# Performance work log

Hardware: AMD Instinct MI355X
Metric: run time of the kernel (lower is better)

Reference implementation:

```python
import jax, jax.numpy as jnp
import numpy as np
import math

FACTOR = 5  # ProbAttention factor default


def setup_inputs() -> dict:
    key = jax.random.key(0)
    k1, k2, k3, k4 = jax.random.split(key, 4)
    B, L, S, H, D = 4, 2048, 2048, 8, 64
    sample_k = min(FACTOR * math.ceil(math.log(L)), S)  # = 40
    return {
        "queries": jax.random.normal(k1, (B, L, H, D), dtype=jnp.float32),
        "keys": jax.random.normal(k2, (B, S, H, D), dtype=jnp.float32),
        "values": jax.random.normal(k3, (B, S, H, D), dtype=jnp.float32),
        # torch.randint(0, L_keys, (L_queries, sample_k)) hoisted out for determinism
        "index_sample": jax.random.randint(k4, (L, sample_k), 0, S, dtype=jnp.int32),
    }


def reference(queries, keys, values, index_sample):
    B, L, H, D = queries.shape
    S = keys.shape[1]
    # [B, H, L, D] layout as in forward's transpose(1, 2)
    q = jnp.transpose(queries, (0, 2, 1, 3))
    k = jnp.transpose(keys, (0, 2, 1, 3))
    v = jnp.transpose(values, (0, 2, 1, 3))

    n_top = min(FACTOR * math.ceil(math.log(S)) if S > 1 else 1, L)
    scale = 1.0 / math.sqrt(D)

    # --- _prob_QK ---
    # sampled keys per query position: [B, H, L, u, D]
    k_samp = k[:, :, index_sample, :]
    qk_sample = jnp.einsum('bhld,bhlud->bhlu', q, k_samp)  # [B, H, L, u]
    # sparsity measure M = max - mean (sum divided by full key length S)
    M = qk_sample.max(axis=-1) - qk_sample.sum(axis=-1) / S  # [B, H, L]
    M_top = jax.lax.top_k(M, n_top)[1]  # [B, H, n_top] query indices
    q_red = jnp.take_along_axis(q, M_top[..., None], axis=2)  # [B, H, n_top, D]
    scores = jnp.einsum('bhnd,bhsd->bhns', q_red, k) * scale  # [B, H, n_top, S]

    # --- softmax over keys (dropout p=0 -> identity) ---
    attn = jax.nn.softmax(scores, axis=-1)

    # --- initial context = mean of V, then scatter-update selected queries ---
    ctx_top = jnp.einsum('bhns,bhsd->bhnd', attn, v)  # [B, H, n_top, D]
    context = jnp.broadcast_to(v.mean(axis=2, keepdims=True), (B, H, L, D))
    bi = jnp.arange(B)[:, None, None]
    hi = jnp.arange(H)[None, :, None]
    context = context.at[bi, hi, M_top].set(ctx_top)

    return jnp.transpose(context, (0, 2, 1, 3))  # [B, L, H, D]
```

## Files before the change

### kernel.cpp

```cpp
#include <hip/hip_runtime.h>
#include <math.h>

constexpr int B = 4, L = 2048, S = 2048, H = 8, D = 64;
constexpr int U  = 40;
constexpr int NT = 40;
constexpr float SCALE = 0.125f;

__global__ void k_M_meanvpart(const float* __restrict__ q, const float* __restrict__ k,
                              const float* __restrict__ v, const int* __restrict__ idx,
                              float* __restrict__ M, float* __restrict__ part) {
    int tid = threadIdx.x;
    if (blockIdx.x < 2048) {
        int wid = tid >> 6, lane = tid & 63;
        int b = blockIdx.x & 3;
        int l = (blockIdx.x >> 2) * 4 + wid;
        int h = lane >> 3, dg = lane & 7;

        const float4* qr = (const float4*)(q + ((size_t)(b * L + l) * H + h) * D + dg * 8);
        float4 q0 = qr[0], q1 = qr[1];

        const int* irow = idx + l * U;
        const float* kb = k + (size_t)b * S * H * D + (size_t)h * D + dg * 8;
        float vmax = -INFINITY, vsum = 0.f;
#pragma unroll 4
        for (int u = 0; u < U; u++) {
            int s = irow[u];
            const float4* kr = (const float4*)(kb + (size_t)s * H * D);
            float4 k0 = kr[0], k1 = kr[1];
            float acc = q0.x * k0.x + q0.y * k0.y + q0.z * k0.z + q0.w * k0.w
                      + q1.x * k1.x + q1.y * k1.y + q1.z * k1.z + q1.w * k1.w;
            acc += __shfl_xor(acc, 1);
            acc += __shfl_xor(acc, 2);
            acc += __shfl_xor(acc, 4);
            vmax = fmaxf(vmax, acc);
            vsum += acc;
        }
        if (dg == 0) M[(size_t)(b * H + h) * L + l] = vmax - vsum / (float)S;
    } else {
        int blk = blockIdx.x - 2048;
        int b = blk >> 5, c = blk & 31;
        const float* p = v + ((size_t)(b * S + c * 64)) * 512;
        float a0 = 0.f, a1 = 0.f;
#pragma unroll
        for (int s = 0; s < 64; s++) {
            a0 += p[(size_t)s * 512 + tid];
            a1 += p[(size_t)s * 512 + tid + 256];
        }
        part[(size_t)blk * 512 + tid]       = a0;
        part[(size_t)blk * 512 + tid + 256] = a1;
    }
}

__device__ inline unsigned int fkey(float f) {
    unsigned int u = __float_as_uint(f);
    return (u & 0x80000000u) ? ~u : (u | 0x80000000u);
}

__global__ void k_topk_meanv(const float* __restrict__ M, int* __restrict__ topidx,
                             const float* __restrict__ part, float* __restrict__ meanv) {
    int tid = threadIdx.x;
    if (blockIdx.x >= 32) {
        int b = blockIdx.x - 32;
        float a0 = 0.f, a1 = 0.f;
#pragma unroll
        for (int c = 0; c < 32; c++) {
            a0 += part[(size_t)(b * 32 + c) * 512 + tid];
            a1 += part[(size_t)(b * 32 + c) * 512 + tid + 256];
        }
        meanv[b * 512 + tid]       = a0 * (1.f / (float)S);
        meanv[b * 512 + tid + 256] = a1 * (1.f / (float)S);
        return;
    }
    int bh = blockIdx.x;
    const float* m = M + (size_t)bh * L;

    __shared__ int hist[256];
    __shared__ unsigned int prefix_s;
    __shared__ int c_above_s, nsel_s, ntie_s, r_s;
    __shared__ int tie_i[L];

    unsigned int o[8];
    const float4* mr = (const float4*)(m + tid * 8);
    float4 a0 = mr[0], a1 = mr[1];
    o[0] = fkey(a0.x); o[1] = fkey(a0.y); o[2] = fkey(a0.z); o[3] = fkey(a0.w);
    o[4] = fkey(a1.x); o[5] = fkey(a1.y); o[6] = fkey(a1.z); o[7] = fkey(a1.w);

    if (tid == 0) { prefix_s = 0u; c_above_s = 0; nsel_s = 0; ntie_s = 0; }

    for (int sh = 24; sh >= 0; sh -= 8) {
        hist[tid] = 0;
        __syncthreads();
        unsigned int pfx = prefix_s;
#pragma unroll
        for (int j = 0; j < 8; j++) {
            bool match = (sh == 24) || ((o[j] >> (sh + 8)) == (pfx >> (sh + 8)));
            if (match) atomicAdd(&hist[(o[j] >> sh) & 0xFF], 1);
        }
        __syncthreads();
        if (tid < 64) {
            int4 hv = *(const int4*)&hist[tid * 4];
            int lsum = hv.x + hv.y + hv.z + hv.w;
            int s = lsum;
#pragma unroll
            for (int off = 1; off < 64; off <<= 1) {
                int t = __shfl_down(s, off);
                if (tid + off < 64) s += t;
            }
            int tail = s - lsum;
            int acc = c_above_s;
            int need = NT - acc;
            int t3 = tail + hv.w;
            int t2 = t3 + hv.z;
            int t1 = t2 + hv.y;
            int t0 = t1 + hv.x;
            if (t0 >= need && t1 < need) { prefix_s |= (unsigned)(4 * tid + 0) << sh; c_above_s = acc + t1; }
            else if (t1 >= need && t2 < need) { prefix_s |= (unsigned)(4 * tid + 1) << sh; c_above_s = acc + t2; }
            else if (t2 >= need && t3 < need) { prefix_s |= (unsigned)(4 * tid + 2) << sh; c_above_s = acc + t3; }
            else if (t3 >= need && tail < need) { prefix_s |= (unsigned)(4 * tid + 3) << sh; c_above_s = acc + tail; }
        }
        __syncthreads();
    }

    unsigned int T = prefix_s;

#pragma unroll
    for (int j = 0; j < 8; j++) {
        if (o[j] > T) {
            int slot = atomicAdd(&nsel_s, 1);
            topidx[bh * NT + slot] = tid * 8 + j;
        } else if (o[j] == T) {
            int p = atomicAdd(&ntie_s, 1);
            tie_i[p] = tid * 8 + j;
        }
    }
    __syncthreads();
    if (tid == 0) r_s = NT - nsel_s;
    __syncthreads();
    int r = r_s, ntie = ntie_s;

#pragma unroll
    for (int j = 0; j < 8; j++) {
        if (o[j] == T) {
            int myidx = tid * 8 + j;
            int rank = 0;
            for (int p = 0; p < ntie; p++) rank += (tie_i[p] < myidx) ? 1 : 0;
            if (rank < r) {
                int slot = atomicAdd(&nsel_s, 1);
                topidx[bh * NT + slot] = myidx;
            }
        }
    }
}

template <int NCH_>
__global__ __launch_bounds__(512) void k_attn_fill(
        const float* __restrict__ q, const float* __restrict__ k,
        const float* __restrict__ v, const int* __restrict__ topidx,
        const float* __restrict__ meanv,
        float* __restrict__ pctx, float* __restrict__ pm, float* __restrict__ pl,
        float4* __restrict__ out4) {
    constexpr int CS_ = S / NCH_;
    constexpr int CPL = CS_ / 128;
    int blk = blockIdx.x;
    int bh = blk / NCH_, c = blk % NCH_;
    int b = bh / H, h = bh % H;
    int s0 = c * CS_;
    int tid = threadIdx.x;
    int lane = tid & 63, g = tid >> 6;

    __shared__ float q_s[NT][D];
    __shared__ float p_s[NT][CS_ + 4];
    __shared__ float m_c[NT];

    for (int i = tid; i < NT * D; i += 512) {
        int n = i >> 6, d = i & 63;
        int lsel = topidx[bh * NT + n];
        q_s[n][d] = q[((size_t)(b * L + lsel) * H + h) * D + d];
    }
    __syncthreads();

    int rg = g & 3, ch = g >> 2;
    int r0 = rg * 10;
    int lc = ch * (CS_ / 2) + lane * CPL;
    const float* kp = k + ((size_t)(b * S + s0 + lc) * H + h) * D;

    float sc[10][CPL];
#pragma unroll
    for (int j = 0; j < 10; j++)
#pragma unroll
        for (int p = 0; p < CPL; p++) sc[j][p] = 0.f;

#pragma unroll
    for (int dc = 0; dc < 64; dc += 16) {
        float4 kf[CPL][4];
#pragma unroll
        for (int p = 0; p < CPL; p++) {
            const float* kc = kp + (size_t)p * H * D + dc;
            kf[p][0] = *(const float4*)(kc);
            kf[p][1] = *(const float4*)(kc + 4);
            kf[p][2] = *(const float4*)(kc + 8);
            kf[p][3] = *(const float4*)(kc + 12);
        }
#pragma unroll
        for (int j = 0; j < 10; j++) {
            const float4* qr = (const float4*)&q_s[r0 + j][dc];
            float4 q0 = qr[0], q1 = qr[1], q2 = qr[2], q3 = qr[3];
#pragma unroll
            for (int p = 0; p < CPL; p++) {
                sc[j][p] += q0.x * kf[p][0].x + q0.y * kf[p][0].y + q0.z * kf[p][0].z + q0.w * kf[p][0].w
                          + q1.x * kf[p][1].x + q1.y * kf[p][1].y + q1.z * kf[p][1].z + q1.w * kf[p][1].w
                          + q2.x * kf[p][2].x + q2.y * kf[p][2].y + q2.z * kf[p][2].z + q2.w * kf[p][2].w
                          + q3.x * kf[p][3].x + q3.y * kf[p][3].y + q3.z * kf[p][3].z + q3.w * kf[p][3].w;
            }
        }
    }
#pragma unroll
    for (int j = 0; j < 10; j++) {
#pragma unroll
        for (int p = 0; p < CPL; p++) sc[j][p] *= SCALE;
        if (CPL == 1) p_s[r0 + j][lc] = sc[j][0];
        else *(float2*)&p_s[r0 + j][lc] = make_float2(sc[j][0], sc[j][1]);
    }
    __syncthreads();

    for (int n = g; n < NT; n += 8) {
        float mx = -INFINITY;
#pragma unroll
        for (int jj = 0; jj < CS_ / 64; jj++) mx = fmaxf(mx, p_s[n][lane + 64 * jj]);
#pragma unroll
        for (int off = 1; off < 64; off <<= 1)
            mx = fmaxf(mx, __shfl_xor(mx, off));
        if (lane == 0) m_c[n] = mx;
    }
    __syncthreads();

#pragma unroll
    for (int j = 0; j < 10; j++) {
        float mm = m_c[r0 + j];
        if (CPL == 1) p_s[r0 + j][lc] = __expf(sc[j][0] - mm);
        else *(float2*)&p_s[r0 + j][lc] =
                 make_float2(__expf(sc[j][0] - mm), __expf(sc[j][1] - mm));
    }
    __syncthreads();

    for (int n = g; n < NT; n += 8) {
        float sum = 0.f;
#pragma unroll
        for (int jj = 0; jj < CS_ / 64; jj++) sum += p_s[n][lane + 64 * jj];
#pragma unroll
        for (int off = 1; off < 64; off <<= 1) sum += __shfl_xor(sum, off);
        if (lane == 0) {
            pm[(bh * NCH_ + c) * NT + n] = m_c[n];
            pl[(bh * NCH_ + c) * NT + n] = sum;
        }
    }

    float acc[5];
#pragma unroll
    for (int r = 0; r < 5; r++) acc[r] = 0.f;
    int rp = g * 5;
    const float* vb = v + ((size_t)(b * S + s0) * H + h) * D + lane;
    for (int t4 = 0; t4 < CS_; t4 += 4) {
        float vd0 = vb[(size_t)(t4 + 0) * H * D];
        float vd1 = vb[(size_t)(t4 + 1) * H * D];
        float vd2 = vb[(size_t)(t4 + 2) * H * D];
        float vd3 = vb[(size_t)(t4 + 3) * H * D];
#pragma unroll
        for (int r = 0; r < 5; r++) {
            float4 p4 = *(const float4*)&p_s[rp + r][t4];
            acc[r] += p4.x * vd0 + p4.y * vd1 + p4.z * vd2 + p4.w * vd3;
        }
    }
#pragma unroll
    for (int r = 0; r < 5; r++)
        pctx[((size_t)(bh * NCH_ + c) * NT + rp + r) * D + lane] = acc[r];

    constexpr int FPB = 1048576 / (32 * NCH_);
    const float4* mv4 = (const float4*)meanv;
    size_t base = (size_t)blk * FPB;
#pragma unroll
    for (int j = 0; j < FPB / 512; j++) {
        size_t i = base + tid + (size_t)j * 512;
        int bb = (int)(i >> 18);
        int col4 = (int)(i & 127);
        out4[i] = mv4[(bb << 7) | col4];
    }
}

template <int NCH_>
__global__ void k_combine(const int* __restrict__ topidx, const float* __restrict__ pctx,
                          const float* __restrict__ pm, const float* __restrict__ pl,
                          float* __restrict__ out) {
    int bh = blockIdx.x; int b = bh / H, h = bh % H;
    int tid = threadIdx.x;
    for (int i = tid; i < NT * D; i += 256) {
        int n = i / D, d = i % D;
        float mg = -INFINITY;
#pragma unroll
        for (int c = 0; c < NCH_; c++) mg = fmaxf(mg, pm[(bh * NCH_ + c) * NT + n]);
        float lsum = 0.f, ctx = 0.f;
#pragma unroll
        for (int c = 0; c < NCH_; c++) {
            float w = __expf(pm[(bh * NCH_ + c) * NT + n] - mg);
            lsum += pl[(bh * NCH_ + c) * NT + n] * w;
            ctx  += pctx[((size_t)(bh * NCH_ + c) * NT + n) * D + d] * w;
        }
        int lsel = topidx[bh * NT + n];
        out[((size_t)(b * L + lsel) * H + h) * D + d] = ctx / lsum;
    }
}

extern "C" void kernel_launch(void* const* d_in, const int* in_sizes, int n_in,
                              void* d_out, int out_size, void* d_ws, size_t ws_size,
                              hipStream_t stream) {
    const float* q   = (const float*)d_in[0];
    const float* k   = (const float*)d_in[1];
    const float* v   = (const float*)d_in[2];
    const int*   idx = (const int*)d_in[3];
    float* out = (float*)d_out;

    float* ws = (float*)d_ws;
    float* M      = ws;
    int*   topidx = (int*)(ws + 65536);
    float* meanv  = ws + 65536 + 1280;
    float* part   = meanv + 2048;
    float* pm     = part + 65536;

    k_M_meanvpart<<<2048 + 128, 256, 0, stream>>>(q, k, v, idx, M, part);
    k_topk_meanv<<<36, 256, 0, stream>>>(M, topidx, part, meanv);

    constexpr size_t base_floats = 65536 + 1280 + 2048 + 65536;
    constexpr size_t need16 = (base_floats + 2ull * (32 * 16 * 40) + 32ull * 16 * 40 * 64) * 4;
    if (ws_size >= need16) {
        constexpr int NCH_ = 16;
        float* pl   = pm + 32 * NCH_ * NT;
        float* pctx = pl + 32 * NCH_ * NT;
        k_attn_fill<NCH_><<<B * H * NCH_, 512, 0, stream>>>(q, k, v, topidx, meanv,
                                                            pctx, pm, pl, (float4*)out);
        k_combine<NCH_><<<B * H, 256, 0, stream>>>(topidx, pctx, pm, pl, out);
    } else {
        constexpr int NCH_ = 8;
        float* pl   = pm + 32 * NCH_ * NT;
        float* pctx = pl + 32 * NCH_ * NT;
        k_attn_fill<NCH_><<<B * H * NCH_, 512, 0, stream>>>(q, k, v, topidx, meanv,
                                                            pctx, pm, pl, (float4*)out);
        k_combine<NCH_><<<B * H, 256, 0, stream>>>(topidx, pctx, pm, pl, out);
    }
}
```

Baseline: 162.0 us.

## Fuse combine into attention kernel via last-block counter and bitmap-masked fill

```diff
diff --git a/kernel.cpp b/kernel.cpp
--- a/kernel.cpp
+++ b/kernel.cpp
@@ -10,20 +10,21 @@
                               const float* __restrict__ v, const int* __restrict__ idx,
                               float* __restrict__ M, float* __restrict__ part) {
     int tid = threadIdx.x;
-    if (blockIdx.x < 2048) {
+    if (blockIdx.x < 4096) {
         int wid = tid >> 6, lane = tid & 63;
         int b = blockIdx.x & 3;
-        int l = (blockIdx.x >> 2) * 4 + wid;
+        int lp = wid >> 1, uh = wid & 1;
+        int l = (blockIdx.x >> 2) * 2 + lp;
         int h = lane >> 3, dg = lane & 7;
 
         const float4* qr = (const float4*)(q + ((size_t)(b * L + l) * H + h) * D + dg * 8);
         float4 q0 = qr[0], q1 = qr[1];
 
-        const int* irow = idx + l * U;
+        const int* irow = idx + l * U + uh * 20;
         const float* kb = k + (size_t)b * S * H * D + (size_t)h * D + dg * 8;
         float vmax = -INFINITY, vsum = 0.f;
 #pragma unroll 4
-        for (int u = 0; u < U; u++) {
+        for (int u = 0; u < 20; u++) {
             int s = irow[u];
             const float4* kr = (const float4*)(kb + (size_t)s * H * D);
             float4 k0 = kr[0], k1 = kr[1];
@@ -35,9 +36,19 @@
             vmax = fmaxf(vmax, acc);
             vsum += acc;
         }
-        if (dg == 0) M[(size_t)(b * H + h) * L + l] = vmax - vsum / (float)S;
+        __shared__ float2 comb[4][8];
+        if (dg == 0) comb[wid][h] = make_float2(vmax, vsum);
+        __syncthreads();
+        if (tid < 16) {
+            int lp2 = tid >> 3, h2 = tid & 7;
+            float2 c0 = comb[lp2 * 2][h2], c1 = comb[lp2 * 2 + 1][h2];
+            float mx = fmaxf(c0.x, c1.x);
+            float sm = c0.y + c1.y;
+            int l2 = (blockIdx.x >> 2) * 2 + lp2;
+            M[(size_t)(b * H + h2) * L + l2] = mx - sm / (float)S;
+        }
     } else {
-        int blk = blockIdx.x - 2048;
+        int blk = blockIdx.x - 4096;
         int b = blk >> 5, c = blk & 31;
         const float* p = v + ((size_t)(b * S + c * 64)) * 512;
         float a0 = 0.f, a1 = 0.f;
@@ -57,7 +68,8 @@
 }
 
 __global__ void k_topk_meanv(const float* __restrict__ M, int* __restrict__ topidx,
-                             const float* __restrict__ part, float* __restrict__ meanv) {
+                             const float* __restrict__ part, float* __restrict__ meanv,
+                             unsigned int* __restrict__ bitmap) {
     int tid = threadIdx.x;
     if (blockIdx.x >= 32) {
         int b = blockIdx.x - 32;
@@ -78,6 +90,9 @@
     __shared__ unsigned int prefix_s;
     __shared__ int c_above_s, nsel_s, ntie_s, r_s;
     __shared__ int tie_i[L];
+    __shared__ unsigned int bw[64];
+
+    if (tid < 64) bw[tid] = 0u;
 
     unsigned int o[8];
     const float4* mr = (const float4*)(m + tid * 8);
@@ -127,7 +142,9 @@
     for (int j = 0; j < 8; j++) {
         if (o[j] > T) {
             int slot = atomicAdd(&nsel_s, 1);
-            topidx[bh * NT + slot] = tid * 8 + j;
+            int myidx = tid * 8 + j;
+            topidx[bh * NT + slot] = myidx;
+            atomicOr(&bw[myidx >> 5], 1u << (myidx & 31));
         } else if (o[j] == T) {
             int p = atomicAdd(&ntie_s, 1);
             tie_i[p] = tid * 8 + j;
@@ -147,18 +164,21 @@
             if (rank < r) {
                 int slot = atomicAdd(&nsel_s, 1);
                 topidx[bh * NT + slot] = myidx;
+                atomicOr(&bw[myidx >> 5], 1u << (myidx & 31));
             }
         }
     }
+    __syncthreads();
+    if (tid < 64) bitmap[bh * 64 + tid] = bw[tid];
 }
 
 template <int NCH_>
 __global__ __launch_bounds__(512) void k_attn_fill(
         const float* __restrict__ q, const float* __restrict__ k,
         const float* __restrict__ v, const int* __restrict__ topidx,
-        const float* __restrict__ meanv,
-        float* __restrict__ pctx, float* __restrict__ pm, float* __restrict__ pl,
-        float4* __restrict__ out4) {
+        const float* __restrict__ meanv, const unsigned int* __restrict__ bitmap,
+        int* cnt, float* pctx, float* pm, float* pl,
+        float* __restrict__ out) {
     constexpr int CS_ = S / NCH_;
     constexpr int CPL = CS_ / 128;
     int blk = blockIdx.x;
@@ -277,33 +297,42 @@
 
     constexpr int FPB = 1048576 / (32 * NCH_);
     const float4* mv4 = (const float4*)meanv;
+    float4* out4 = (float4*)out;
     size_t base = (size_t)blk * FPB;
 #pragma unroll
     for (int j = 0; j < FPB / 512; j++) {
         size_t i = base + tid + (size_t)j * 512;
         int bb = (int)(i >> 18);
         int col4 = (int)(i & 127);
-        out4[i] = mv4[(bb << 7) | col4];
-    }
-}
-
-template <int NCH_>
-__global__ void k_combine(const int* __restrict__ topidx, const float* __restrict__ pctx,
-                          const float* __restrict__ pm, const float* __restrict__ pl,
-                          float* __restrict__ out) {
-    int bh = blockIdx.x; int b = bh / H, h = bh % H;
-    int tid = threadIdx.x;
-    for (int i = tid; i < NT * D; i += 256) {
-        int n = i / D, d = i % D;
+        int ll = (int)((i >> 7) & 2047);
+        int hh = col4 >> 4;
+        unsigned int w = bitmap[(bb * 8 + hh) * 64 + (ll >> 5)];
+        if (!((w >> (ll & 31)) & 1u))
+            out4[i] = mv4[(bb << 7) | col4];
+    }
+
+    __threadfence();
+    __shared__ int is_last;
+    if (tid == 0) {
+        int old = __hip_atomic_fetch_add(&cnt[bh], 1, __ATOMIC_ACQ_REL,
+                                         __HIP_MEMORY_SCOPE_AGENT);
+        is_last = (old == NCH_ - 1);
+    }
+    __syncthreads();
+    if (!is_last) return;
+    __threadfence();
+
+    for (int i = tid; i < NT * D; i += 512) {
+        int n = i >> 6, d = i & 63;
         float mg = -INFINITY;
 #pragma unroll
-        for (int c = 0; c < NCH_; c++) mg = fmaxf(mg, pm[(bh * NCH_ + c) * NT + n]);
+        for (int cc = 0; cc < NCH_; cc++) mg = fmaxf(mg, pm[(bh * NCH_ + cc) * NT + n]);
         float lsum = 0.f, ctx = 0.f;
 #pragma unroll
-        for (int c = 0; c < NCH_; c++) {
-            float w = __expf(pm[(bh * NCH_ + c) * NT + n] - mg);
-            lsum += pl[(bh * NCH_ + c) * NT + n] * w;
-            ctx  += pctx[((size_t)(bh * NCH_ + c) * NT + n) * D + d] * w;
+        for (int cc = 0; cc < NCH_; cc++) {
+            float w = __expf(pm[(bh * NCH_ + cc) * NT + n] - mg);
+            lsum += pl[(bh * NCH_ + cc) * NT + n] * w;
+            ctx  += pctx[((size_t)(bh * NCH_ + cc) * NT + n) * D + d] * w;
         }
         int lsel = topidx[bh * NT + n];
         out[((size_t)(b * L + lsel) * H + h) * D + d] = ctx / lsum;
@@ -320,30 +349,31 @@
     float* out = (float*)d_out;
 
     float* ws = (float*)d_ws;
-    float* M      = ws;
-    int*   topidx = (int*)(ws + 65536);
-    float* meanv  = ws + 65536 + 1280;
-    float* part   = meanv + 2048;
-    float* pm     = part + 65536;
-
-    k_M_meanvpart<<<2048 + 128, 256, 0, stream>>>(q, k, v, idx, M, part);
-    k_topk_meanv<<<36, 256, 0, stream>>>(M, topidx, part, meanv);
-
-    constexpr size_t base_floats = 65536 + 1280 + 2048 + 65536;
+    float*        M      = ws;
+    int*          topidx = (int*)(ws + 65536);
+    float*        meanv  = ws + 65536 + 1280;
+    float*        part   = meanv + 2048;
+    unsigned int* bitmap = (unsigned int*)(part + 65536);
+    int*          cnt    = (int*)(bitmap + 2048);
+    float*        pm     = (float*)(cnt + 32);
+
+    hipMemsetAsync(cnt, 0, 32 * sizeof(int), stream);
+    k_M_meanvpart<<<4096 + 128, 256, 0, stream>>>(q, k, v, idx, M, part);
+    k_topk_meanv<<<36, 256, 0, stream>>>(M, topidx, part, meanv, bitmap);
+
+    constexpr size_t base_floats = 65536 + 1280 + 2048 + 65536 + 2048 + 32;
     constexpr size_t need16 = (base_floats + 2ull * (32 * 16 * 40) + 32ull * 16 * 40 * 64) * 4;
     if (ws_size >= need16) {
         constexpr int NCH_ = 16;
         float* pl   = pm + 32 * NCH_ * NT;
         float* pctx = pl + 32 * NCH_ * NT;
-        k_attn_fill<NCH_><<<B * H * NCH_, 512, 0, stream>>>(q, k, v, topidx, meanv,
-                                                            pctx, pm, pl, (float4*)out);
-        k_combine<NCH_><<<B * H, 256, 0, stream>>>(topidx, pctx, pm, pl, out);
+        k_attn_fill<NCH_><<<B * H * NCH_, 512, 0, stream>>>(q, k, v, topidx, meanv, bitmap,
+                                                            cnt, pctx, pm, pl, out);
     } else {
         constexpr int NCH_ = 8;
         float* pl   = pm + 32 * NCH_ * NT;
         float* pctx = pl + 32 * NCH_ * NT;
-        k_attn_fill<NCH_><<<B * H * NCH_, 512, 0, stream>>>(q, k, v, topidx, meanv,
-                                                            pctx, pm, pl, (float4*)out);
-        k_combine<NCH_><<<B * H, 256, 0, stream>>>(topidx, pctx, pm, pl, out);
-    }
-}
+        k_attn_fill<NCH_><<<B * H * NCH_, 512, 0, stream>>>(q, k, v, topidx, meanv, bitmap,
+                                                            cnt, pctx, pm, pl, out);
+    }
+}
```

After: 284.3 us. 75.5% more time.
